# Kernel optimization log

Measured on AMD Instinct MI355X. Metric: run time of the kernel, lower is better.

## Reference

```python
import jax, jax.numpy as jnp
import numpy as np

N_NODES = 50000
N_EDGES = 800000
N_GLOBALS = 64
DX, DE, DU = 128, 32, 32
HID, OUT = 128, 128
EPS = 1e-5


def _mlp(x, W1, b1, W2, b2, g, b):
    # Linear -> ReLU -> Linear -> ReLU (activate_final) -> LayerNorm (normalize)
    h = jax.nn.relu(x @ W1 + b1)
    h = jax.nn.relu(h @ W2 + b2)
    mu = jnp.mean(h, axis=-1, keepdims=True)
    var = jnp.var(h, axis=-1, keepdims=True)
    return g * (h - mu) * jax.lax.rsqrt(var + EPS) + b


def _mlp_params(key, d_in):
    k1, k2 = jax.random.split(key)
    W1 = jax.random.normal(k1, (d_in, HID), jnp.float32) / np.sqrt(d_in)
    b1 = jnp.zeros((HID,), jnp.float32)
    W2 = jax.random.normal(k2, (HID, OUT), jnp.float32) / np.sqrt(HID)
    b2 = jnp.zeros((OUT,), jnp.float32)
    g = jnp.ones((OUT,), jnp.float32)
    b = jnp.zeros((OUT,), jnp.float32)
    return W1, b1, W2, b2, g, b


def setup_inputs() -> dict:
    key = jax.random.key(0)
    ks = jax.random.split(key, 8)
    x = jax.random.normal(ks[0], (N_NODES, DX), jnp.float32)
    e = jax.random.normal(ks[1], (N_EDGES, DE), jnp.float32)
    u = jax.random.normal(ks[2], (N_GLOBALS, DU), jnp.float32)
    edge_index = jax.random.randint(ks[3], (2, N_EDGES), 0, N_NODES, jnp.int64 if jax.config.jax_enable_x64 else jnp.int32)
    batch = jnp.sort(jax.random.randint(ks[4], (N_NODES,), 0, N_GLOBALS))
    # edge MLP in: e(32) + recv(128) + send(128) + u(32) = 320
    eW1, eb1, eW2, eb2, eg, ebt = _mlp_params(ks[5], DE + DX + DX + DU)
    # node MLP in: x(128) + edge_aggr(128) + u(32) = 288
    nW1, nb1, nW2, nb2, ng, nbt = _mlp_params(ks[6], DX + OUT + DU)
    # global MLP in: u(32) + node_aggr(128) + edge_aggr(128) = 288
    gW1, gb1, gW2, gb2, gg, gbt = _mlp_params(ks[7], DU + OUT + OUT)
    return dict(x=x, e=e, u=u, edge_index=edge_index, batch=batch,
                eW1=eW1, eb1=eb1, eW2=eW2, eb2=eb2, eg=eg, ebt=ebt,
                nW1=nW1, nb1=nb1, nW2=nW2, nb2=nb2, ng=ng, nbt=nbt,
                gW1=gW1, gb1=gb1, gW2=gW2, gb2=gb2, gg=gg, gbt=gbt)


def reference(x, e, u, edge_index, batch,
              eW1, eb1, eW2, eb2, eg, ebt,
              nW1, nb1, nW2, nb2, ng, nbt,
              gW1, gb1, gW2, gb2, gg, gbt):
    row, col = edge_index[0], edge_index[1]
    edge_batch = batch[row]  # graph id per edge

    # --- EdgeModel: concat(edge, receiver, sender, global->edges) -> MLP ---
    edge_in = jnp.concatenate([e, x[col], x[row], u[edge_batch]], axis=1)
    e2 = _mlp(edge_in, eW1, eb1, eW2, eb2, eg, ebt)  # [N_EDGES, OUT]

    # --- NodeModel: concat(node, edges->node via receiver, global->nodes) -> MLP ---
    edge_to_node = jax.ops.segment_sum(e2, col, num_segments=N_NODES)
    node_in = jnp.concatenate([x, edge_to_node, u[batch]], axis=1)
    x2 = _mlp(node_in, nW1, nb1, nW2, nb2, ng, nbt)  # [N_NODES, OUT]

    # --- GlobalModel: concat(global, nodes->global, edges->global) -> MLP ---
    node_to_glob = jax.ops.segment_sum(x2, batch, num_segments=N_GLOBALS)
    edge_to_glob = jax.ops.segment_sum(e2, edge_batch, num_segments=N_GLOBALS)
    glob_in = jnp.concatenate([u, node_to_glob, edge_to_glob], axis=1)
    u2 = _mlp(glob_in, gW1, gb1, gW2, gb2, gg, gbt)  # [N_GLOBALS, OUT]

    return x2, e2, u2
```

## Files before the change

### kernel.cpp

```cpp
#include <hip/hip_runtime.h>
#include <hip/hip_bf16.h>

typedef __attribute__((ext_vector_type(8))) short bf16x8;
typedef __attribute__((ext_vector_type(4))) float f32x4;

#define EPSV 1e-5f
#define NN 50000
#define NE 800000
#define NG 64
#define SEGB 1000
#define MFMA16(a, b, c) __builtin_amdgcn_mfma_f32_16x16x32_bf16(a, b, c, 0, 0, 0)

__device__ __forceinline__ unsigned short f2bf(float f) {
  union { float f; unsigned u; } v; v.f = f;
  unsigned r = v.u + 0x7FFFu + ((v.u >> 16) & 1u);
  return (unsigned short)(r >> 16);
}
__device__ __forceinline__ float bf2f(unsigned short h) {
  union { unsigned u; float f; } v; v.u = ((unsigned)h) << 16;
  return v.f;
}


__global__ __launch_bounds__(256) void cvt_vec_kernel(
    const float* __restrict__ x, unsigned short* __restrict__ xb) {
  const int NX4 = (NN * 128) / 4;
  for (int idx = blockIdx.x * 256 + threadIdx.x; idx < NX4;
       idx += gridDim.x * 256) {
    float4 v = ((const float4*)x)[idx];
    ushort4 o;
    o.x = f2bf(v.x); o.y = f2bf(v.y); o.z = f2bf(v.z); o.w = f2bf(v.w);
    ((ushort4*)xb)[idx] = o;
  }
}

__global__ __launch_bounds__(256) void cvt_small_kernel(
    const float* __restrict__ u,
    const float* __restrict__ eW1, const float* __restrict__ eW2,
    const float* __restrict__ nW1, const float* __restrict__ nW2,
    unsigned short* __restrict__ ub,
    unsigned short* __restrict__ W1eT, unsigned short* __restrict__ WpqT,
    unsigned short* __restrict__ eW2T,
    unsigned short* __restrict__ nW1T, unsigned short* __restrict__ nW2T,
    float* __restrict__ Rg) {
  int i = blockIdx.x * 256 + threadIdx.x;
  const int R0 = NG * 32;
  const int R1 = R0 + 128 * 32;
  const int R2 = R1 + 256 * 128;
  const int R3 = R2 + 128 * 128;
  const int R4 = R3 + 128 * 320;
  const int R5 = R4 + 128 * 128;
  const int R6 = R5 + NG * 128;
  if (i < R0) {
    ub[i] = f2bf(u[i]);
  } else if (i < R1) {
    int j = i - R0; int n = j >> 5, k = j & 31;
    W1eT[j] = f2bf(eW1[k * 128 + n]);
  } else if (i < R2) {
    int j = i - R1; int n = j >> 7, k = j & 127;
    WpqT[j] = (n < 128) ? f2bf(eW1[(32 + k) * 128 + n])
                        : f2bf(eW1[(160 + k) * 128 + (n - 128)]);
  } else if (i < R3) {
    int j = i - R2; int n = j >> 7, k = j & 127;
    eW2T[j] = f2bf(eW2[k * 128 + n]);
  } else if (i < R4) {
    int j = i - R3; int n = j / 320, k = j % 320;
    nW1T[j] = (k < 288) ? f2bf(nW1[k * 128 + n]) : (unsigned short)0;
  } else if (i < R5) {
    int j = i - R4; int n = j >> 7, k = j & 127;
    nW2T[j] = f2bf(nW2[k * 128 + n]);
  } else if (i < R6) {
    int j = i - R5; int g = j >> 7, n = j & 127;
    float s = 0.f;
#pragma unroll
    for (int k = 0; k < 32; ++k) s += u[g * 32 + k] * eW1[(288 + k) * 128 + n];
    Rg[j] = s;
  }
}

__global__ __launch_bounds__(256, 2) void pq_kernel(
    const unsigned short* __restrict__ xb,
    const unsigned short* __restrict__ WpqT,
    unsigned short* __restrict__ PQ) {
  __shared__ __align__(16) unsigned short Asm[64][136];
  __shared__ __align__(16) unsigned short Bsm[256][72];
  const int tid = threadIdx.x;
  {
    const int r = tid >> 2, q = tid & 3;
    const int grow = blockIdx.x * 64 + r;
    const uint4 zero = {0u, 0u, 0u, 0u};
    if (grow < NN) {
      const uint4* xs = (const uint4*)(xb + (size_t)grow * 128 + q * 32);
#pragma unroll
      for (int k = 0; k < 4; ++k) *(uint4*)&Asm[r][q * 32 + k * 8] = xs[k];
    } else {
#pragma unroll
      for (int k = 0; k < 4; ++k) *(uint4*)&Asm[r][q * 32 + k * 8] = zero;
    }
  }
  const int w = tid >> 6, lane = tid & 63;
  const int l15 = lane & 15, lg = lane >> 4;
  f32x4 acc[16];
#pragma unroll
  for (int ni = 0; ni < 16; ++ni) acc[ni] = f32x4{0.f, 0.f, 0.f, 0.f};
  for (int kc = 0; kc < 2; ++kc) {
    {
      const uint4* src = (const uint4*)(WpqT + (size_t)tid * 128 + kc * 64);
#pragma unroll
      for (int k = 0; k < 8; ++k) *(uint4*)&Bsm[tid][k * 8] = src[k];
    }
    __syncthreads();
    bf16x8 a0 = *(bf16x8*)&Asm[w * 16 + l15][kc * 64 + lg * 8];
    bf16x8 a1 = *(bf16x8*)&Asm[w * 16 + l15][kc * 64 + 32 + lg * 8];
#pragma unroll
    for (int ni = 0; ni < 16; ++ni) {
      bf16x8 b0 = *(bf16x8*)&Bsm[ni * 16 + l15][lg * 8];
      bf16x8 b1 = *(bf16x8*)&Bsm[ni * 16 + l15][32 + lg * 8];
      acc[ni] = MFMA16(a0, b0, acc[ni]);
      acc[ni] = MFMA16(a1, b1, acc[ni]);
    }
    __syncthreads();
  }
  unsigned short (*Cl)[264] = (unsigned short(*)[264])&Bsm[0][0];
#pragma unroll
  for (int ni = 0; ni < 16; ++ni)
#pragma unroll
    for (int reg = 0; reg < 4; ++reg)
      Cl[w * 16 + lg * 4 + reg][l15 + ni * 16] = f2bf(acc[ni][reg]);
  __syncthreads();
  {
    const int r = tid >> 2, q = tid & 3;
    const int grow = blockIdx.x * 64 + r;
    if (grow < NN) {
#pragma unroll
      for (int k = 0; k < 8; ++k)
        *(uint4*)(PQ + (size_t)grow * 256 + q * 64 + k * 8) =
            *(uint4*)&Cl[r][q * 64 + k * 8];
    }
  }
}


__global__ __launch_bounds__(256) void pre_kernel(
    const int* __restrict__ rowIdx, const int* __restrict__ colIdx,
    int* __restrict__ cnt_r, int* __restrict__ cnt_s) {
  int i = blockIdx.x * 256 + threadIdx.x;
  if (i < NE) {
    atomicAdd(&cnt_r[colIdx[i]], 1);
    atomicAdd(&cnt_s[rowIdx[i]], 1);
  }
}

__global__ __launch_bounds__(1024) void scan2_kernel(
    const int* __restrict__ cnt_r, int* __restrict__ offs_r, int* __restrict__ cur_r,
    const int* __restrict__ cnt_s, int* __restrict__ offs_s, int* __restrict__ cur_s) {
  __shared__ int sums[1024];
  const int* cnt = blockIdx.x ? cnt_s : cnt_r;
  int* offs = blockIdx.x ? offs_s : offs_r;
  int* cur  = blockIdx.x ? cur_s : cur_r;
  const int t = threadIdx.x;
  const int base = t * 49;
  int s = 0;
  for (int j = 0; j < 49; ++j) {
    int idx = base + j;
    if (idx < NN) s += cnt[idx];
  }
  sums[t] = s;
  __syncthreads();
  for (int off = 1; off < 1024; off <<= 1) {
    int add = (t >= off) ? sums[t - off] : 0;
    __syncthreads();
    sums[t] += add;
    __syncthreads();
  }
  int run = (t == 0) ? 0 : sums[t - 1];
  for (int j = 0; j < 49; ++j) {
    int idx = base + j;
    if (idx < NN) {
      offs[idx] = run; cur[idx] = run;
      run += cnt[idx];
    }
  }
}

__global__ __launch_bounds__(256) void fill_both_kernel(
    const int* __restrict__ rowIdx, const int* __restrict__ colIdx,
    const int* __restrict__ batch,
    int* __restrict__ cur_r, int* __restrict__ cur_s,
    int* __restrict__ eidlist_r, int* __restrict__ eidlist_s,
    int* __restrict__ gs) {
  int i = blockIdx.x * 256 + threadIdx.x;
  if (i < NE) {
    const int c = colIdx[i];
    const int p = atomicAdd(&cur_r[c], 1);
    eidlist_r[p] = i;
    const int r = rowIdx[i];
    const int p2 = atomicAdd(&cur_s[r], 1);
    eidlist_s[p2] = i;
    gs[p2] = batch[r];
  }
}

__global__ __launch_bounds__(256, 3) void edge_kernel(
    const float* __restrict__ ef,
    const unsigned short* __restrict__ PQ,
    const float* __restrict__ Rg,
    const int* __restrict__ rowI, const int* __restrict__ colI,
    const int* __restrict__ batch,
    const unsigned short* __restrict__ W1eT,
    const unsigned short* __restrict__ W2T,
    const float* __restrict__ b1, const float* __restrict__ b2,
    const float* __restrict__ gam, const float* __restrict__ bet,
    float* __restrict__ outE) {
  __shared__ __align__(16) char U[27648];
  __shared__ __align__(16) unsigned short Hsm[64][136];
  __shared__ float cb1[128], cb2[128], cg[128], cbt[128];
  unsigned short (*B1e)[40] = (unsigned short(*)[40])U;
  unsigned short (*Ssm)[136] = (unsigned short(*)[136])(U + 10240);
  unsigned short (*Bsm)[72] = (unsigned short(*)[72])U;

  const int tid = threadIdx.x;
  const int base = blockIdx.x * 64;
  if (tid < 128) {
    cb1[tid] = b1[tid]; cb2[tid] = b2[tid];
    cg[tid] = gam[tid]; cbt[tid] = bet[tid];
    const uint4* s = (const uint4*)(W1eT + tid * 32);
#pragma unroll
    for (int k = 0; k < 4; ++k) *(uint4*)&B1e[tid][k * 8] = s[k];
  }

  {
    const int r = tid >> 2, q = tid & 3;
    const int grow = base + r;
    const int rcv = colI[grow];
    const int snd = rowI[grow];
    const int g = batch[snd];
    const unsigned short* pp = PQ + (size_t)rcv * 256 + q * 32;
    const unsigned short* qq = PQ + (size_t)snd * 256 + 128 + q * 32;
    const float* rr = Rg + g * 128 + q * 32;
#pragma unroll
    for (int k = 0; k < 8; ++k) {
      ushort4 pv = *(const ushort4*)(pp + k * 4);
      ushort4 qv = *(const ushort4*)(qq + k * 4);
      float4 rv = *(const float4*)(rr + k * 4);
      ushort4 o;
      o.x = f2bf(bf2f(pv.x) + bf2f(qv.x) + rv.x);
      o.y = f2bf(bf2f(pv.y) + bf2f(qv.y) + rv.y);
      o.z = f2bf(bf2f(pv.z) + bf2f(qv.z) + rv.z);
      o.w = f2bf(bf2f(pv.w) + bf2f(qv.w) + rv.w);
      *(ushort4*)&Ssm[r][q * 32 + k * 4] = o;
    }
  }
  __syncthreads();

  const int w = tid >> 6, lane = tid & 63;
  const int l15 = lane & 15, lg = lane >> 4;

  f32x4 acc[8];
#pragma unroll
  for (int ni = 0; ni < 8; ++ni) acc[ni] = f32x4{0.f, 0.f, 0.f, 0.f};
  {
    const int arow = base + w * 16 + l15;
    const float* ep = ef + (size_t)arow * 32 + lg * 8;
    float4 v0 = *(const float4*)ep;
    float4 v1 = *(const float4*)(ep + 4);
    bf16x8 a;
    a[0] = (short)f2bf(v0.x); a[1] = (short)f2bf(v0.y);
    a[2] = (short)f2bf(v0.z); a[3] = (short)f2bf(v0.w);
    a[4] = (short)f2bf(v1.x); a[5] = (short)f2bf(v1.y);
    a[6] = (short)f2bf(v1.z); a[7] = (short)f2bf(v1.w);
#pragma unroll
    for (int ni = 0; ni < 8; ++ni) {
      bf16x8 b0 = *(bf16x8*)&B1e[ni * 16 + l15][lg * 8];
      acc[ni] = MFMA16(a, b0, acc[ni]);
    }
  }

#pragma unroll
  for (int ni = 0; ni < 8; ++ni) {
    const int ncol = l15 + ni * 16;
    const float bias = cb1[ncol];
#pragma unroll
    for (int reg = 0; reg < 4; ++reg) {
      const int mrow = w * 16 + lg * 4 + reg;
      const float sv = bf2f(Ssm[mrow][ncol]);
      Hsm[mrow][ncol] = f2bf(fmaxf(acc[ni][reg] + sv + bias, 0.f));
    }
  }
  __syncthreads();

  f32x4 acc2[8];
#pragma unroll
  for (int ni = 0; ni < 8; ++ni) acc2[ni] = f32x4{0.f, 0.f, 0.f, 0.f};
  for (int kc = 0; kc < 2; ++kc) {
    {
      const int n = tid >> 1, half = tid & 1;
      const uint4* src = (const uint4*)(W2T + (size_t)n * 128 + kc * 64 + half * 32);
#pragma unroll
      for (int k = 0; k < 4; ++k)
        *(uint4*)&Bsm[n][half * 32 + k * 8] = src[k];
    }
    __syncthreads();
    bf16x8 a0 = *(bf16x8*)&Hsm[w * 16 + l15][kc * 64 + lg * 8];
    bf16x8 a1 = *(bf16x8*)&Hsm[w * 16 + l15][kc * 64 + 32 + lg * 8];
#pragma unroll
    for (int ni = 0; ni < 8; ++ni) {
      bf16x8 b0 = *(bf16x8*)&Bsm[ni * 16 + l15][lg * 8];
      bf16x8 b1 = *(bf16x8*)&Bsm[ni * 16 + l15][32 + lg * 8];
      acc2[ni] = MFMA16(a0, b0, acc2[ni]);
      acc2[ni] = MFMA16(a1, b1, acc2[ni]);
    }
    __syncthreads();
  }

  float hv[8][4];
  float sreg[4] = {0.f, 0.f, 0.f, 0.f}, ssreg[4] = {0.f, 0.f, 0.f, 0.f};
#pragma unroll
  for (int ni = 0; ni < 8; ++ni) {
    const int ncol = l15 + ni * 16;
    const float bias = cb2[ncol];
#pragma unroll
    for (int reg = 0; reg < 4; ++reg) {
      const float h = fmaxf(acc2[ni][reg] + bias, 0.f);
      hv[ni][reg] = h;
      sreg[reg] += h; ssreg[reg] += h * h;
    }
  }
#pragma unroll
  for (int reg = 0; reg < 4; ++reg) {
    float s = sreg[reg], ss = ssreg[reg];
#pragma unroll
    for (int off = 1; off < 16; off <<= 1) {
      s += __shfl_xor(s, off, 64);
      ss += __shfl_xor(ss, off, 64);
    }
    sreg[reg] = s; ssreg[reg] = ss;
  }
#pragma unroll
  for (int reg = 0; reg < 4; ++reg) {
    const int grow = base + w * 16 + lg * 4 + reg;
    const float mu = sreg[reg] * (1.f / 128.f);
    const float var = ssreg[reg] * (1.f / 128.f) - mu * mu;
    const float rstd = rsqrtf(var + EPSV);
#pragma unroll
    for (int ni = 0; ni < 8; ++ni) {
      const int ncol = l15 + ni * 16;
      const float y = cg[ncol] * (hv[ni][reg] - mu) * rstd + cbt[ncol];
      outE[(size_t)grow * 128 + ncol] = y;
    }
  }
}

__global__ __launch_bounds__(256, 2) void post_kernel(
    const float* __restrict__ outE,
    const int* __restrict__ eidl_s, const int* __restrict__ gsA,
    float* __restrict__ e2g,
    const unsigned short* __restrict__ xb,
    const unsigned short* __restrict__ ub,
    const int* __restrict__ batch,
    const int* __restrict__ offs, const int* __restrict__ cnt,
    const int* __restrict__ eidlist,
    const unsigned short* __restrict__ W1T,
    const unsigned short* __restrict__ W2T,
    const float* __restrict__ b1, const float* __restrict__ b2,
    const float* __restrict__ gam, const float* __restrict__ bet,
    float* __restrict__ outX, float* __restrict__ n2g) {
  __shared__ __align__(16) char U[50176];
  __shared__ __align__(16) unsigned short Bsm[128][72];
  __shared__ float cb1[128], cb2[128], cg[128], cbt[128];

  const int tid = threadIdx.x;

  if (blockIdx.x < SEGB) {
    const int c4 = (tid & 31) * 4;
    const int sub = tid >> 5;
    const int start = blockIdx.x * 800;
    int gcur = gsA[start + sub];
    float4 acc = {0.f, 0.f, 0.f, 0.f};
    for (int it = 0; it < 25; ++it) {
      const int pbase = start + sub + it * 32;
      int eid[4], g[4];
#pragma unroll
      for (int j = 0; j < 4; ++j) {
        eid[j] = eidl_s[pbase + j * 8];
        g[j]   = gsA[pbase + j * 8];
      }
      float4 v[4];
#pragma unroll
      for (int j = 0; j < 4; ++j)
        v[j] = *(const float4*)(outE + (size_t)eid[j] * 128 + c4);
#pragma unroll
      for (int j = 0; j < 4; ++j) {
        if (g[j] != gcur) {
          atomicAdd(&e2g[gcur * 128 + c4],     acc.x);
          atomicAdd(&e2g[gcur * 128 + c4 + 1], acc.y);
          atomicAdd(&e2g[gcur * 128 + c4 + 2], acc.z);
          atomicAdd(&e2g[gcur * 128 + c4 + 3], acc.w);
          gcur = g[j]; acc = float4{0.f, 0.f, 0.f, 0.f};
        }
        acc.x += v[j].x; acc.y += v[j].y; acc.z += v[j].z; acc.w += v[j].w;
      }
    }
    atomicAdd(&e2g[gcur * 128 + c4],     acc.x);
    atomicAdd(&e2g[gcur * 128 + c4 + 1], acc.y);
    atomicAdd(&e2g[gcur * 128 + c4 + 2], acc.z);
    atomicAdd(&e2g[gcur * 128 + c4 + 3], acc.w);
    return;
  }

  const int bx = blockIdx.x - SEGB;
  unsigned short (*Asm)[328] = (unsigned short(*)[328])U;
  unsigned short (*Hsm)[136] = (unsigned short(*)[136])U;
  float* bins = (float*)(U + 17408);

  if (tid < 128) {
    cb1[tid] = b1[tid]; cb2[tid] = b2[tid];
    cg[tid] = gam[tid]; cbt[tid] = bet[tid];
  }

  {
    const int r = tid >> 2, q = tid & 3;
    const int grow = bx * 64 + r;
    const bool valid = grow < NN;
    const uint4 zero = {0u, 0u, 0u, 0u};
    if (valid) {
      const uint4* xs = (const uint4*)(xb + (size_t)grow * 128 + q * 32);
#pragma unroll
      for (int k = 0; k < 4; ++k) *(uint4*)&Asm[r][q * 32 + k * 8] = xs[k];
    } else {
#pragma unroll
      for (int k = 0; k < 4; ++k) *(uint4*)&Asm[r][q * 32 + k * 8] = zero;
    }
    float4 a[8];
#pragma unroll
    for (int k = 0; k < 8; ++k) a[k] = float4{0.f, 0.f, 0.f, 0.f};
    if (valid) {
      const int start = offs[grow];
      const int deg = cnt[grow];
      int j = 0;
      for (; j + 2 <= deg; j += 2) {
        const int e0 = eidlist[start + j], e1 = eidlist[start + j + 1];
        const float4* s0 = (const float4*)(outE + (size_t)e0 * 128 + q * 32);
        const float4* s1 = (const float4*)(outE + (size_t)e1 * 128 + q * 32);
#pragma unroll
        for (int k = 0; k < 8; ++k) {
          float4 v0 = s0[k], v1 = s1[k];
          a[k].x += v0.x + v1.x; a[k].y += v0.y + v1.y;
          a[k].z += v0.z + v1.z; a[k].w += v0.w + v1.w;
        }
      }
      if (j < deg) {
        const int e0 = eidlist[start + j];
        const float4* s0 = (const float4*)(outE + (size_t)e0 * 128 + q * 32);
#pragma unroll
        for (int k = 0; k < 8; ++k) {
          float4 v0 = s0[k];
          a[k].x += v0.x; a[k].y += v0.y; a[k].z += v0.z; a[k].w += v0.w;
        }
      }
    }
#pragma unroll
    for (int k = 0; k < 8; ++k) {
      ushort4 o;
      o.x = f2bf(a[k].x); o.y = f2bf(a[k].y);
      o.z = f2bf(a[k].z); o.w = f2bf(a[k].w);
      *(ushort4*)&Asm[r][128 + q * 32 + k * 4] = o;
    }
    const int g = valid ? batch[grow] : 0;
    uint4 uv = valid ? *(const uint4*)(ub + g * 32 + q * 8) : zero;
    *(uint4*)&Asm[r][256 + q * 8] = uv;
    *(uint4*)&Asm[r][288 + q * 8] = zero;
  }

  const int w = tid >> 6;
  const int lane = tid & 63;
  const int l15 = lane & 15, lg = lane >> 4;

  f32x4 acc[8];
#pragma unroll
  for (int ni = 0; ni < 8; ++ni) acc[ni] = f32x4{0.f, 0.f, 0.f, 0.f};

  for (int kc = 0; kc < 5; ++kc) {
    {
      const int n = tid >> 1, half = tid & 1;
      const uint4* src = (const uint4*)(W1T + (size_t)n * 320 + kc * 64 + half * 32);
#pragma unroll
      for (int k = 0; k < 4; ++k)
        *(uint4*)&Bsm[n][half * 32 + k * 8] = src[k];
    }
    __syncthreads();
    bf16x8 a0 = *(bf16x8*)&Asm[w * 16 + l15][kc * 64 + lg * 8];
    bf16x8 a1 = *(bf16x8*)&Asm[w * 16 + l15][kc * 64 + 32 + lg * 8];
#pragma unroll
    for (int ni = 0; ni < 8; ++ni) {
      bf16x8 bb0 = *(bf16x8*)&Bsm[ni * 16 + l15][lg * 8];
      bf16x8 bb1 = *(bf16x8*)&Bsm[ni * 16 + l15][32 + lg * 8];
      acc[ni] = MFMA16(a0, bb0, acc[ni]);
      acc[ni] = MFMA16(a1, bb1, acc[ni]);
    }
    __syncthreads();
  }

#pragma unroll
  for (int ni = 0; ni < 8; ++ni) {
    const int ncol = l15 + ni * 16;
    const float bias = cb1[ncol];
#pragma unroll
    for (int reg = 0; reg < 4; ++reg) {
      const int mrow = w * 16 + lg * 4 + reg;
      Hsm[mrow][ncol] = f2bf(fmaxf(acc[ni][reg] + bias, 0.f));
    }
  }
  for (int i = tid; i < NG * 128; i += 256) bins[i] = 0.f;

  f32x4 acc2[8];
#pragma unroll
  for (int ni = 0; ni < 8; ++ni) acc2[ni] = f32x4{0.f, 0.f, 0.f, 0.f};
  for (int kc = 0; kc < 2; ++kc) {
    {
      const int n = tid >> 1, half = tid & 1;
      const uint4* src = (const uint4*)(W2T + (size_t)n * 128 + kc * 64 + half * 32);
#pragma unroll
      for (int k = 0; k < 4; ++k)
        *(uint4*)&Bsm[n][half * 32 + k * 8] = src[k];
    }
    __syncthreads();
    bf16x8 a0 = *(bf16x8*)&Hsm[w * 16 + l15][kc * 64 + lg * 8];
    bf16x8 a1 = *(bf16x8*)&Hsm[w * 16 + l15][kc * 64 + 32 + lg * 8];
#pragma unroll
    for (int ni = 0; ni < 8; ++ni) {
      bf16x8 bb0 = *(bf16x8*)&Bsm[ni * 16 + l15][lg * 8];
      bf16x8 bb1 = *(bf16x8*)&Bsm[ni * 16 + l15][32 + lg * 8];
      acc2[ni] = MFMA16(a0, bb0, acc2[ni]);
      acc2[ni] = MFMA16(a1, bb1, acc2[ni]);
    }
    __syncthreads();
  }

  float hv[8][4];
  float sreg[4] = {0.f, 0.f, 0.f, 0.f}, ssreg[4] = {0.f, 0.f, 0.f, 0.f};
#pragma unroll
  for (int ni = 0; ni < 8; ++ni) {
    const int ncol = l15 + ni * 16;
    const float bias = cb2[ncol];
#pragma unroll
    for (int reg = 0; reg < 4; ++reg) {
      const float h = fmaxf(acc2[ni][reg] + bias, 0.f);
      hv[ni][reg] = h;
      sreg[reg] += h; ssreg[reg] += h * h;
    }
  }
#pragma unroll
  for (int reg = 0; reg < 4; ++reg) {
    float s = sreg[reg], ss = ssreg[reg];
#pragma unroll
    for (int off = 1; off < 16; off <<= 1) {
      s += __shfl_xor(s, off, 64);
      ss += __shfl_xor(ss, off, 64);
    }
    sreg[reg] = s; ssreg[reg] = ss;
  }
#pragma unroll
  for (int reg = 0; reg < 4; ++reg) {
    const int mrow = w * 16 + lg * 4 + reg;
    const int grow = bx * 64 + mrow;
    if (grow >= NN) continue;
    const float mu = sreg[reg] * (1.f / 128.f);
    const float var = ssreg[reg] * (1.f / 128.f) - mu * mu;
    const float rstd = rsqrtf(var + EPSV);
    const int g = batch[grow];
#pragma unroll
    for (int ni = 0; ni < 8; ++ni) {
      const int ncol = l15 + ni * 16;
      const float y = cg[ncol] * (hv[ni][reg] - mu) * rstd + cbt[ncol];
      outX[(size_t)grow * 128 + ncol] = y;
      atomicAdd(&bins[g * 128 + ncol], y);
    }
  }
  __syncthreads();
  const int first = bx * 64;
  const int last = min(first + 63, NN - 1);
  const int gmin = batch[first], gmax = batch[last];
  const int cntf = (gmax - gmin + 1) * 128;
  for (int i = tid; i < cntf; i += 256)
    atomicAdd(&n2g[gmin * 128 + i], bins[gmin * 128 + i]);
}

__global__ __launch_bounds__(128) void glob_kernel(
    const float* __restrict__ u, const float* __restrict__ n2g,
    const float* __restrict__ e2g,
    const float* __restrict__ gW1, const float* __restrict__ gb1,
    const float* __restrict__ gW2, const float* __restrict__ gb2,
    const float* __restrict__ gg, const float* __restrict__ gbt,
    float* __restrict__ outU) {
  __shared__ float in[288];
  __shared__ float h1[128];
  __shared__ float red[4];
  const int g = blockIdx.x, t = threadIdx.x;
  if (t < 32) in[t] = u[g * 32 + t];
  in[32 + t] = n2g[g * 128 + t];
  in[160 + t] = e2g[g * 128 + t];
  __syncthreads();
  float a = gb1[t];
  for (int k = 0; k < 288; ++k) a += in[k] * gW1[k * 128 + t];
  h1[t] = fmaxf(a, 0.f);
  __syncthreads();
  float h = gb2[t];
  for (int k = 0; k < 128; ++k) h += h1[k] * gW2[k * 128 + t];
  h = fmaxf(h, 0.f);
  float s = h, ss = h * h;
  for (int off = 1; off < 64; off <<= 1) {
    s += __shfl_xor(s, off, 64);
    ss += __shfl_xor(ss, off, 64);
  }
  if ((t & 63) == 0) { red[(t >> 6) * 2] = s; red[(t >> 6) * 2 + 1] = ss; }
  __syncthreads();
  const float S = red[0] + red[2], SS = red[1] + red[3];
  const float mu = S * (1.f / 128.f);
  const float var = SS * (1.f / 128.f) - mu * mu;
  const float rstd = rsqrtf(var + EPSV);
  outU[g * 128 + t] = gg[t] * (h - mu) * rstd + gbt[t];
}

extern "C" void kernel_launch(void* const* d_in, const int* in_sizes, int n_in,
                              void* d_out, int out_size, void* d_ws,
                              size_t ws_size, hipStream_t stream) {
  const float* x   = (const float*)d_in[0];
  const float* e   = (const float*)d_in[1];
  const float* u   = (const float*)d_in[2];
  const int* eidx  = (const int*)d_in[3];
  const int* batch = (const int*)d_in[4];
  const float* eW1 = (const float*)d_in[5];
  const float* eb1 = (const float*)d_in[6];
  const float* eW2 = (const float*)d_in[7];
  const float* eb2 = (const float*)d_in[8];
  const float* eg  = (const float*)d_in[9];
  const float* ebt = (const float*)d_in[10];
  const float* nW1 = (const float*)d_in[11];
  const float* nb1 = (const float*)d_in[12];
  const float* nW2 = (const float*)d_in[13];
  const float* nb2 = (const float*)d_in[14];
  const float* ng  = (const float*)d_in[15];
  const float* nbt = (const float*)d_in[16];
  const float* gW1 = (const float*)d_in[17];
  const float* gb1 = (const float*)d_in[18];
  const float* gW2 = (const float*)d_in[19];
  const float* gb2 = (const float*)d_in[20];
  const float* gg  = (const float*)d_in[21];
  const float* gbt = (const float*)d_in[22];

  char* ws = (char*)d_ws;
  float* e2g           = (float*)(ws + 0);
  float* n2g           = (float*)(ws + 32768);
  int*   cnt_r         = (int*)  (ws + 65536);
  int*   cnt_s         = (int*)  (ws + 265536);
  int*   offs_r        = (int*)  (ws + 465536);
  int*   cur_r         = (int*)  (ws + 665536);
  int*   offs_s        = (int*)  (ws + 865536);
  int*   cur_s         = (int*)  (ws + 1065536);
  int*   eidlist_r     = (int*)  (ws + 1265536);
  int*   eidlist_s     = (int*)  (ws + 4465536);
  int*   gs            = (int*)  (ws + 7665536);
  unsigned short* xb   = (unsigned short*)(ws + 10865536);
  unsigned short* ub   = (unsigned short*)(ws + 23665536);
  unsigned short* W1eT = (unsigned short*)(ws + 23669632);
  unsigned short* WpqT = (unsigned short*)(ws + 23677824);
  unsigned short* eW2T = (unsigned short*)(ws + 23743360);
  unsigned short* nW1T = (unsigned short*)(ws + 23776128);
  unsigned short* nW2T = (unsigned short*)(ws + 23858048);
  unsigned short* PQ   = (unsigned short*)(ws + 23890816);
  float* Rg            = (float*)(ws + 49490816);

  hipMemsetAsync(ws, 0, 465536, stream);

  cvt_vec_kernel<<<1024, 256, 0, stream>>>(x, xb);
  cvt_small_kernel<<<472, 256, 0, stream>>>(u, eW1, eW2, nW1, nW2, ub, W1eT,
                                            WpqT, eW2T, nW1T, nW2T, Rg);
  pq_kernel<<<(NN + 63) / 64, 256, 0, stream>>>(xb, WpqT, PQ);

  float* outX = (float*)d_out;
  float* outE = outX + (size_t)NN * 128;
  float* outU = outE + (size_t)NE * 128;

  const int* rowI = eidx;
  const int* colI = eidx + NE;

  pre_kernel<<<(NE + 255) / 256, 256, 0, stream>>>(rowI, colI, cnt_r, cnt_s);
  scan2_kernel<<<2, 1024, 0, stream>>>(cnt_r, offs_r, cur_r,
                                       cnt_s, offs_s, cur_s);
  fill_both_kernel<<<(NE + 255) / 256, 256, 0, stream>>>(
      rowI, colI, batch, cur_r, cur_s, eidlist_r, eidlist_s, gs);

  edge_kernel<<<NE / 64, 256, 0, stream>>>(e, PQ, Rg, rowI, colI, batch,
                                           W1eT, eW2T, eb1, eb2, eg, ebt,
                                           outE);
  post_kernel<<<SEGB + (NN + 63) / 64, 256, 0, stream>>>(
      outE, eidlist_s, gs, e2g,
      xb, ub, batch, offs_r, cnt_r, eidlist_r,
      nW1T, nW2T, nb1, nb2, ng, nbt, outX, n2g);
  glob_kernel<<<NG, 128, 0, stream>>>(u, n2g, e2g, gW1, gb1, gW2, gb2, gg, gbt,
                                      outU);
}
```

Measured before the change: 828.3 us.

## Shrink post_kernel LDS footprint to fit three blocks per CU

Cuts shared memory in the node-MLP path. The padded 320-wide A tile becomes a 256-wide tile plus a separate 32-wide global-feature tile, the weight staging buffer shrinks to 32-column K chunks (9 and 4 iterations instead of 5 and 2), and the per-block graph bins shrink from 64 to 8 graphs. Blocks spanning 8 or more graphs fall back to direct global atomics. The goal is to raise launch bounds to 3 blocks per CU for more latency hiding, at the cost of more K-loop iterations and barriers.

```diff
diff --git a/kernel.cpp b/kernel.cpp
--- a/kernel.cpp
+++ b/kernel.cpp
@@ -351,7 +351,7 @@
   }
 }
 
-__global__ __launch_bounds__(256, 2) void post_kernel(
+__global__ __launch_bounds__(256, 3) void post_kernel(
     const float* __restrict__ outE,
     const int* __restrict__ eidl_s, const int* __restrict__ gsA,
     float* __restrict__ e2g,
@@ -365,8 +365,9 @@
     const float* __restrict__ b1, const float* __restrict__ b2,
     const float* __restrict__ gam, const float* __restrict__ bet,
     float* __restrict__ outX, float* __restrict__ n2g) {
-  __shared__ __align__(16) char U[50176];
-  __shared__ __align__(16) unsigned short Bsm[128][72];
+  __shared__ __align__(16) char U[33792];
+  __shared__ __align__(16) unsigned short Usm[64][40];
+  __shared__ __align__(16) unsigned short Bsm[128][40];
   __shared__ float cb1[128], cb2[128], cg[128], cbt[128];
 
   const int tid = threadIdx.x;
@@ -409,7 +410,7 @@
   }
 
   const int bx = blockIdx.x - SEGB;
-  unsigned short (*Asm)[328] = (unsigned short(*)[328])U;
+  unsigned short (*Asm)[264] = (unsigned short(*)[264])U;
   unsigned short (*Hsm)[136] = (unsigned short(*)[136])U;
   float* bins = (float*)(U + 17408);
 
@@ -417,6 +418,10 @@
     cb1[tid] = b1[tid]; cb2[tid] = b2[tid];
     cg[tid] = gam[tid]; cbt[tid] = bet[tid];
   }
+
+  const int gmin = batch[bx * 64];
+  const int gmax = batch[min(bx * 64 + 63, NN - 1)];
+  const bool fastbins = (gmax - gmin) < 8;
 
   {
     const int r = tid >> 2, q = tid & 3;
@@ -468,8 +473,7 @@
     }
     const int g = valid ? batch[grow] : 0;
     uint4 uv = valid ? *(const uint4*)(ub + g * 32 + q * 8) : zero;
-    *(uint4*)&Asm[r][256 + q * 8] = uv;
-    *(uint4*)&Asm[r][288 + q * 8] = zero;
+    *(uint4*)&Usm[r][q * 8] = uv;
   }
 
   const int w = tid >> 6;
@@ -480,23 +484,20 @@
 #pragma unroll
   for (int ni = 0; ni < 8; ++ni) acc[ni] = f32x4{0.f, 0.f, 0.f, 0.f};
 
-  for (int kc = 0; kc < 5; ++kc) {
+  for (int kc = 0; kc < 9; ++kc) {
     {
       const int n = tid >> 1, half = tid & 1;
-      const uint4* src = (const uint4*)(W1T + (size_t)n * 320 + kc * 64 + half * 32);
-#pragma unroll
-      for (int k = 0; k < 4; ++k)
-        *(uint4*)&Bsm[n][half * 32 + k * 8] = src[k];
-    }
-    __syncthreads();
-    bf16x8 a0 = *(bf16x8*)&Asm[w * 16 + l15][kc * 64 + lg * 8];
-    bf16x8 a1 = *(bf16x8*)&Asm[w * 16 + l15][kc * 64 + 32 + lg * 8];
+      const uint4* src = (const uint4*)(W1T + (size_t)n * 320 + kc * 32 + half * 16);
+      *(uint4*)&Bsm[n][half * 16] = src[0];
+      *(uint4*)&Bsm[n][half * 16 + 8] = src[1];
+    }
+    __syncthreads();
+    bf16x8 a0 = (kc < 8) ? *(bf16x8*)&Asm[w * 16 + l15][kc * 32 + lg * 8]
+                         : *(bf16x8*)&Usm[w * 16 + l15][lg * 8];
 #pragma unroll
     for (int ni = 0; ni < 8; ++ni) {
-      bf16x8 bb0 = *(bf16x8*)&Bsm[ni * 16 + l15][lg * 8];
-      bf16x8 bb1 = *(bf16x8*)&Bsm[ni * 16 + l15][32 + lg * 8];
-      acc[ni] = MFMA16(a0, bb0, acc[ni]);
-      acc[ni] = MFMA16(a1, bb1, acc[ni]);
+      bf16x8 bb = *(bf16x8*)&Bsm[ni * 16 + l15][lg * 8];
+      acc[ni] = MFMA16(a0, bb, acc[ni]);
     }
     __syncthreads();
   }
@@ -511,28 +512,24 @@
       Hsm[mrow][ncol] = f2bf(fmaxf(acc[ni][reg] + bias, 0.f));
     }
   }
-  for (int i = tid; i < NG * 128; i += 256) bins[i] = 0.f;
+  for (int i = tid; i < 8 * 128; i += 256) bins[i] = 0.f;
 
   f32x4 acc2[8];
 #pragma unroll
   for (int ni = 0; ni < 8; ++ni) acc2[ni] = f32x4{0.f, 0.f, 0.f, 0.f};
-  for (int kc = 0; kc < 2; ++kc) {
+  for (int kc = 0; kc < 4; ++kc) {
     {
       const int n = tid >> 1, half = tid & 1;
-      const uint4* src = (const uint4*)(W2T + (size_t)n * 128 + kc * 64 + half * 32);
-#pragma unroll
-      for (int k = 0; k < 4; ++k)
-        *(uint4*)&Bsm[n][half * 32 + k * 8] = src[k];
-    }
-    __syncthreads();
-    bf16x8 a0 = *(bf16x8*)&Hsm[w * 16 + l15][kc * 64 + lg * 8];
-    bf16x8 a1 = *(bf16x8*)&Hsm[w * 16 + l15][kc * 64 + 32 + lg * 8];
+      const uint4* src = (const uint4*)(W2T + (size_t)n * 128 + kc * 32 + half * 16);
+      *(uint4*)&Bsm[n][half * 16] = src[0];
+      *(uint4*)&Bsm[n][half * 16 + 8] = src[1];
+    }
+    __syncthreads();
+    bf16x8 a0 = *(bf16x8*)&Hsm[w * 16 + l15][kc * 32 + lg * 8];
 #pragma unroll
     for (int ni = 0; ni < 8; ++ni) {
-      bf16x8 bb0 = *(bf16x8*)&Bsm[ni * 16 + l15][lg * 8];
-      bf16x8 bb1 = *(bf16x8*)&Bsm[ni * 16 + l15][32 + lg * 8];
-      acc2[ni] = MFMA16(a0, bb0, acc2[ni]);
-      acc2[ni] = MFMA16(a1, bb1, acc2[ni]);
+      bf16x8 bb = *(bf16x8*)&Bsm[ni * 16 + l15][lg * 8];
+      acc2[ni] = MFMA16(a0, bb, acc2[ni]);
     }
     __syncthreads();
   }
@@ -574,16 +571,16 @@
       const int ncol = l15 + ni * 16;
       const float y = cg[ncol] * (hv[ni][reg] - mu) * rstd + cbt[ncol];
       outX[(size_t)grow * 128 + ncol] = y;
-      atomicAdd(&bins[g * 128 + ncol], y);
-    }
-  }
-  __syncthreads();
-  const int first = bx * 64;
-  const int last = min(first + 63, NN - 1);
-  const int gmin = batch[first], gmax = batch[last];
-  const int cntf = (gmax - gmin + 1) * 128;
-  for (int i = tid; i < cntf; i += 256)
-    atomicAdd(&n2g[gmin * 128 + i], bins[gmin * 128 + i]);
+      if (fastbins) atomicAdd(&bins[(g - gmin) * 128 + ncol], y);
+      else          atomicAdd(&n2g[g * 128 + ncol], y);
+    }
+  }
+  if (fastbins) {
+    __syncthreads();
+    const int cntf = (gmax - gmin + 1) * 128;
+    for (int i = tid; i < cntf; i += 256)
+      atomicAdd(&n2g[gmin * 128 + i], bins[i]);
+  }
 }
 
 __global__ __launch_bounds__(128) void glob_kernel(
```

Result: no change. 842.4 us (+1.7%).
